# Kernel optimization log

Hardware: AMD Instinct MI355X
Metric: run time of the kernel (lower is better)

Reference implementation:

```python
import jax, jax.numpy as jnp
from jax import lax
import numpy as np


def _rnn_tanh_layer(x, W_ih, W_hh, b_ih, b_hh, return_seq):
    # x: [B, T, I]; W_ih: [H, I]; W_hh: [H, H]
    B = x.shape[0]
    H = W_hh.shape[0]
    # Precompute input projection for all timesteps (one big GEMM).
    xw = jnp.einsum('bti,hi->bth', x, W_ih) + b_ih + b_hh  # [B, T, H]
    xw_t = jnp.swapaxes(xw, 0, 1)  # [T, B, H] for scan
    h0 = jnp.zeros((B, H), dtype=x.dtype)

    def step(h, xt):
        h_new = jnp.tanh(xt + h @ W_hh.T)
        return h_new, (h_new if return_seq else None)

    hT, hs = lax.scan(step, h0, xw_t)
    if return_seq:
        return jnp.swapaxes(hs, 0, 1), hT  # [B, T, H], [B, H]
    return None, hT


def setup_inputs() -> dict:
    key = jax.random.key(0)
    ks = jax.random.split(key, 12)
    B, T, I, H1, H2, C = 512, 1024, 32, 128, 64, 10

    def unif(k, shape, fan):
        bound = 1.0 / np.sqrt(fan)
        return jax.random.uniform(k, shape, jnp.float32, -bound, bound)

    return {
        'x': jax.random.normal(ks[0], (B, T, I), jnp.float32),
        'W_ih1': unif(ks[1], (H1, I), H1),
        'W_hh1': unif(ks[2], (H1, H1), H1),
        'b_ih1': unif(ks[3], (H1,), H1),
        'b_hh1': unif(ks[4], (H1,), H1),
        'W_ih2': unif(ks[5], (H2, H1), H2),
        'W_hh2': unif(ks[6], (H2, H2), H2),
        'b_ih2': unif(ks[7], (H2,), H2),
        'b_hh2': unif(ks[8], (H2,), H2),
        'W_fc': unif(ks[9], (C, H2), H2),
        'b_fc': unif(ks[10], (C,), H2),
    }


def reference(x, W_ih1, W_hh1, b_ih1, b_hh1, W_ih2, W_hh2, b_ih2, b_hh2, W_fc, b_fc):
    out1, _h1 = _rnn_tanh_layer(x, W_ih1, W_hh1, b_ih1, b_hh1, return_seq=True)
    _none, h2 = _rnn_tanh_layer(out1, W_ih2, W_hh2, b_ih2, b_hh2, return_seq=False)
    # Dropout(p=0.3) is identity in eval mode.
    logits = h2 @ W_fc.T + b_fc  # [B, 10]
    return logits
```

## Files before the change

### kernel.cpp

```cpp
#include <hip/hip_runtime.h>
#include <stdint.h>


typedef _Float16 f16x8 __attribute__((ext_vector_type(8)));
typedef float f32x4 __attribute__((ext_vector_type(4)));

#define MFMA_F16(A, B, C) __builtin_amdgcn_mfma_f32_16x16x32_f16((A), (B), (C), 0, 0, 0)

__device__ __forceinline__ float tanh_fast(float x) {
  float t = __builtin_amdgcn_exp2f(x * 2.88539008177792681472f);
  return 1.0f - 2.0f * __builtin_amdgcn_rcpf(t + 1.0f);
}

__device__ __forceinline__ uint32_t pk16(float a, float b) {
  return __builtin_bit_cast(uint32_t, __builtin_amdgcn_cvt_pkrtz(a, b));
}

__global__ __launch_bounds__(256) void rnn_fused(
    const float* __restrict__ x,
    const float* __restrict__ Wih1, const float* __restrict__ Whh1,
    const float* __restrict__ bih1, const float* __restrict__ bhh1,
    const float* __restrict__ Wih2, const float* __restrict__ Whh2,
    const float* __restrict__ bih2, const float* __restrict__ bhh2,
    const float* __restrict__ Wfc,  const float* __restrict__ bfc,
    float* __restrict__ out)
{
  constexpr int T = 1024, I = 32, H1 = 128, H2 = 64, BB = 16;

  __shared__ __align__(16) unsigned char smem[16384];

  const int tid  = threadIdx.x;
  const int w    = tid >> 6;
  const int lane = tid & 63;
  const int g    = lane >> 4;
  const int n    = lane & 15;
  const int b0   = blockIdx.x * BB;

  {
    uint32_t* p = (uint32_t*)smem;
    for (int i = tid; i < 1024; i += 256) p[i] = 0u;
    uint32_t* q = (uint32_t*)(smem + 8192);
    for (int i = tid; i < 512; i += 256) q[i] = 0u;
  }

  auto cvt8 = [](const float* s) -> f16x8 {
    f16x8 r;
#pragma unroll
    for (int j = 0; j < 8; ++j) r[j] = (_Float16)s[j];
    return r;
  };

  f16x8 aU[2][4];
  f16x8 aI1[2];
  f16x8 aI2[4];
  f16x8 aR2[2];
#pragma unroll
  for (int ti = 0; ti < 2; ++ti) {
    const int ch = (2 * w + ti) * 16 + n;
#pragma unroll
    for (int k4 = 0; k4 < 4; ++k4)
      aU[ti][k4] = cvt8(Whh1 + ch * H1 + k4 * 32 + g * 8);
    aI1[ti] = cvt8(Wih1 + ch * I + g * 8);
  }
  {
    const int ch2 = w * 16 + n;
#pragma unroll
    for (int k4 = 0; k4 < 4; ++k4)
      aI2[k4] = cvt8(Wih2 + ch2 * H1 + k4 * 32 + g * 8);
#pragma unroll
    for (int k2 = 0; k2 < 2; ++k2)
      aR2[k2] = cvt8(Whh2 + ch2 * H2 + k2 * 32 + g * 8);
  }

  f32x4 bias1[2], bias2;
#pragma unroll
  for (int ti = 0; ti < 2; ++ti) {
    const int ch = (2 * w + ti) * 16 + g * 4;
#pragma unroll
    for (int r = 0; r < 4; ++r) bias1[ti][r] = bih1[ch + r] + bhh1[ch + r];
  }
  {
    const int ch2 = w * 16 + g * 4;
#pragma unroll
    for (int r = 0; r < 4; ++r) bias2[r] = bih2[ch2 + r] + bhh2[ch2 + r];
  }

  int roff1[4], roff2[2], woff1[2], woff2;
#pragma unroll
  for (int k4 = 0; k4 < 4; ++k4)
    roff1[k4] = n * 256 + (((k4 * 4 + g) ^ (n & 7)) << 4);
#pragma unroll
  for (int k2 = 0; k2 < 2; ++k2)
    roff2[k2] = n * 128 + (((k2 * 4 + g) ^ (n & 7)) << 4);
#pragma unroll
  for (int ti = 0; ti < 2; ++ti) {
    const int tt = 2 * w + ti;
    woff1[ti] = n * 256 + (((2 * tt + (g >> 1)) ^ (n & 7)) << 4) + (g & 1) * 8;
  }
  woff2 = n * 128 + (((2 * w + (g >> 1)) ^ (n & 7)) << 4) + (g & 1) * 8;

  const float* xp = x + (size_t)(b0 + n) * T * I + g * 8;
  f32x4 xrA0 = *(const f32x4*)(xp + 0 * I);
  f32x4 xrA1 = *(const f32x4*)(xp + 0 * I + 4);
  f32x4 xrB0 = *(const f32x4*)(xp + 1 * I);
  f32x4 xrB1 = *(const f32x4*)(xp + 1 * I + 4);

  __syncthreads();

  auto tanh_pack = [&](const f32x4& a, uint32_t& lo, uint32_t& hi) {
    const float v0 = tanh_fast(a[0]), v1 = tanh_fast(a[1]);
    const float v2 = tanh_fast(a[2]), v3 = tanh_fast(a[3]);
    lo = pk16(v0, v1);
    hi = pk16(v2, v3);
  };

  auto step = [&](int t, int cur, f32x4& xr0, f32x4& xr1) {
    f16x8 xf;
    {
      union { uint32_t u[4]; f16x8 v; } tmp;
      tmp.u[0] = pk16(xr0[0], xr0[1]);
      tmp.u[1] = pk16(xr0[2], xr0[3]);
      tmp.u[2] = pk16(xr1[0], xr1[1]);
      tmp.u[3] = pk16(xr1[2], xr1[3]);
      xf = tmp.v;
    }

    const char* H1c = (const char*)smem + cur * 4096;
    char*       H1n = (char*)smem + (cur ^ 1) * 4096;
    const char* H2r = (const char*)smem + 8192 + (cur ^ 1) * 2048;
    char*       H2w = (char*)smem + 8192 + cur * 2048;

    f16x8 b1[4];
#pragma unroll
    for (int k4 = 0; k4 < 4; ++k4)
      b1[k4] = *(const f16x8*)(H1c + roff1[k4]);

    f32x4 acc0 = bias1[0];
    f32x4 acc1 = bias1[1];
    acc0 = MFMA_F16(aI1[0], xf, acc0);
    acc1 = MFMA_F16(aI1[1], xf, acc1);
#pragma unroll
    for (int k4 = 0; k4 < 4; ++k4) {
      acc0 = MFMA_F16(aU[0][k4], b1[k4], acc0);
      acc1 = MFMA_F16(aU[1][k4], b1[k4], acc1);
    }

    if (t + 2 < T) {
      xr0 = *(const f32x4*)(xp + (t + 2) * I);
      xr1 = *(const f32x4*)(xp + (t + 2) * I + 4);
    }

    if (t > 0) {
      f16x8 b2[2];
#pragma unroll
      for (int k2 = 0; k2 < 2; ++k2)
        b2[k2] = *(const f16x8*)(H2r + roff2[k2]);
      f32x4 acc2 = bias2;
#pragma unroll
      for (int k4 = 0; k4 < 4; ++k4) acc2 = MFMA_F16(aI2[k4], b1[k4], acc2);
#pragma unroll
      for (int k2 = 0; k2 < 2; ++k2) acc2 = MFMA_F16(aR2[k2], b2[k2], acc2);
      uint32_t lo, hi;
      tanh_pack(acc2, lo, hi);
      *(uint2*)(H2w + woff2) = make_uint2(lo, hi);
    }

    {
      uint32_t lo, hi;
      tanh_pack(acc0, lo, hi);
      *(uint2*)(H1n + woff1[0]) = make_uint2(lo, hi);
      tanh_pack(acc1, lo, hi);
      *(uint2*)(H1n + woff1[1]) = make_uint2(lo, hi);
    }

    __syncthreads();
  };

  for (int t2 = 0; t2 < T; t2 += 2) {
    step(t2,     0, xrA0, xrA1);
    step(t2 + 1, 1, xrB0, xrB1);
  }

  {
    const char* H1c = (const char*)smem;
    const char* H2r = (const char*)smem + 8192 + 2048;
    f16x8 b1[4];
#pragma unroll
    for (int k4 = 0; k4 < 4; ++k4)
      b1[k4] = *(const f16x8*)(H1c + roff1[k4]);
    f16x8 b2[2];
#pragma unroll
    for (int k2 = 0; k2 < 2; ++k2)
      b2[k2] = *(const f16x8*)(H2r + roff2[k2]);
    f32x4 acc2 = bias2;
#pragma unroll
    for (int k4 = 0; k4 < 4; ++k4) acc2 = MFMA_F16(aI2[k4], b1[k4], acc2);
#pragma unroll
    for (int k2 = 0; k2 < 2; ++k2) acc2 = MFMA_F16(aR2[k2], b2[k2], acc2);

    f32x4 hv;
#pragma unroll
    for (int r = 0; r < 4; ++r) hv[r] = tanh_fast(acc2[r]);
    const int ch0 = w * 16 + g * 4;
    *(f32x4*)(smem + 12288 + n * 256 + ch0 * 4) = hv;
  }
  __syncthreads();

  if (tid < BB * 10) {
    const int b = tid / 10, c = tid % 10;
    const float* hrow = (const float*)(smem + 12288 + b * 256);
    float acc = bfc[c];
#pragma unroll 8
    for (int k = 0; k < 64; ++k) acc += hrow[k] * Wfc[c * 64 + k];
    out[(size_t)(b0 + b) * 10 + c] = acc;
  }
}

extern "C" void kernel_launch(void* const* d_in, const int* in_sizes, int n_in,
                              void* d_out, int out_size, void* d_ws, size_t ws_size,
                              hipStream_t stream) {
  const float* x    = (const float*)d_in[0];
  const float* Wih1 = (const float*)d_in[1];
  const float* Whh1 = (const float*)d_in[2];
  const float* bih1 = (const float*)d_in[3];
  const float* bhh1 = (const float*)d_in[4];
  const float* Wih2 = (const float*)d_in[5];
  const float* Whh2 = (const float*)d_in[6];
  const float* bih2 = (const float*)d_in[7];
  const float* bhh2 = (const float*)d_in[8];
  const float* Wfc  = (const float*)d_in[9];
  const float* bfc  = (const float*)d_in[10];

  hipLaunchKernelGGL(rnn_fused, dim3(512 / 16), dim3(256), 0, stream,
                     x, Wih1, Whh1, bih1, bhh1, Wih2, Whh2, bih2, bhh2,
                     Wfc, bfc, (float*)d_out);
}
```

Before: 515.1 us.

## Split layer-1 and layer-2 recurrences across warp-specialized wavefronts with lighter barriers

The block grows from 4 to 12 wavefronts. Eight wavefronts each own 16 layer-1 channels and four own 16 layer-2 channels, so each wave's serial MFMA chain per timestep is shorter. Each step now ends with a bare lgkmcnt wait plus s_barrier instead of __syncthreads. The accumulation is split into independent MFMA chains that are summed at the end, and the next timestep's input projection is computed ahead of time off the critical path. The cost is a barrier spanning three times as many waves and higher register/occupancy pressure from 768-thread blocks.

New measurement: 551.6 us. 7.1% more time.

```diff
diff --git a/kernel.cpp b/kernel.cpp
--- a/kernel.cpp
+++ b/kernel.cpp
@@ -16,7 +16,11 @@
   return __builtin_bit_cast(uint32_t, __builtin_amdgcn_cvt_pkrtz(a, b));
 }
 
-__global__ __launch_bounds__(256) void rnn_fused(
+__device__ __forceinline__ void sync_lds() {
+  asm volatile("s_waitcnt lgkmcnt(0)\n\ts_barrier" ::: "memory");
+}
+
+__global__ __launch_bounds__(768) void rnn_fused(
     const float* __restrict__ x,
     const float* __restrict__ Wih1, const float* __restrict__ Whh1,
     const float* __restrict__ bih1, const float* __restrict__ bhh1,
@@ -38,9 +42,9 @@
 
   {
     uint32_t* p = (uint32_t*)smem;
-    for (int i = tid; i < 1024; i += 256) p[i] = 0u;
+    for (int i = tid; i < 1024; i += 768) p[i] = 0u;
     uint32_t* q = (uint32_t*)(smem + 8192);
-    for (int i = tid; i < 512; i += 256) q[i] = 0u;
+    for (int i = tid; i < 512; i += 768) q[i] = 0u;
   }
 
   auto cvt8 = [](const float* s) -> f16x8 {
@@ -50,160 +54,149 @@
     return r;
   };
 
-  f16x8 aU[2][4];
-  f16x8 aI1[2];
-  f16x8 aI2[4];
-  f16x8 aR2[2];
-#pragma unroll
-  for (int ti = 0; ti < 2; ++ti) {
-    const int ch = (2 * w + ti) * 16 + n;
-#pragma unroll
-    for (int k4 = 0; k4 < 4; ++k4)
-      aU[ti][k4] = cvt8(Whh1 + ch * H1 + k4 * 32 + g * 8);
-    aI1[ti] = cvt8(Wih1 + ch * I + g * 8);
-  }
-  {
-    const int ch2 = w * 16 + n;
-#pragma unroll
-    for (int k4 = 0; k4 < 4; ++k4)
-      aI2[k4] = cvt8(Wih2 + ch2 * H1 + k4 * 32 + g * 8);
-#pragma unroll
-    for (int k2 = 0; k2 < 2; ++k2)
-      aR2[k2] = cvt8(Whh2 + ch2 * H2 + k2 * 32 + g * 8);
-  }
-
-  f32x4 bias1[2], bias2;
-#pragma unroll
-  for (int ti = 0; ti < 2; ++ti) {
-    const int ch = (2 * w + ti) * 16 + g * 4;
-#pragma unroll
-    for (int r = 0; r < 4; ++r) bias1[ti][r] = bih1[ch + r] + bhh1[ch + r];
-  }
-  {
-    const int ch2 = w * 16 + g * 4;
-#pragma unroll
-    for (int r = 0; r < 4; ++r) bias2[r] = bih2[ch2 + r] + bhh2[ch2 + r];
-  }
-
-  int roff1[4], roff2[2], woff1[2], woff2;
+  int roff1[4];
 #pragma unroll
   for (int k4 = 0; k4 < 4; ++k4)
     roff1[k4] = n * 256 + (((k4 * 4 + g) ^ (n & 7)) << 4);
-#pragma unroll
-  for (int k2 = 0; k2 < 2; ++k2)
-    roff2[k2] = n * 128 + (((k2 * 4 + g) ^ (n & 7)) << 4);
-#pragma unroll
-  for (int ti = 0; ti < 2; ++ti) {
-    const int tt = 2 * w + ti;
-    woff1[ti] = n * 256 + (((2 * tt + (g >> 1)) ^ (n & 7)) << 4) + (g & 1) * 8;
-  }
-  woff2 = n * 128 + (((2 * w + (g >> 1)) ^ (n & 7)) << 4) + (g & 1) * 8;
-
-  const float* xp = x + (size_t)(b0 + n) * T * I + g * 8;
-  f32x4 xrA0 = *(const f32x4*)(xp + 0 * I);
-  f32x4 xrA1 = *(const f32x4*)(xp + 0 * I + 4);
-  f32x4 xrB0 = *(const f32x4*)(xp + 1 * I);
-  f32x4 xrB1 = *(const f32x4*)(xp + 1 * I + 4);
 
   __syncthreads();
 
-  auto tanh_pack = [&](const f32x4& a, uint32_t& lo, uint32_t& hi) {
-    const float v0 = tanh_fast(a[0]), v1 = tanh_fast(a[1]);
-    const float v2 = tanh_fast(a[2]), v3 = tanh_fast(a[3]);
-    lo = pk16(v0, v1);
-    hi = pk16(v2, v3);
-  };
-
-  auto step = [&](int t, int cur, f32x4& xr0, f32x4& xr1) {
-    f16x8 xf;
+  if (w < 8) {
+    f16x8 aU[4], aI1;
+#pragma unroll
+    for (int k4 = 0; k4 < 4; ++k4)
+      aU[k4] = cvt8(Whh1 + (16 * w + n) * H1 + k4 * 32 + g * 8);
+    aI1 = cvt8(Wih1 + (16 * w + n) * I + g * 8);
+    f32x4 bias1;
+#pragma unroll
+    for (int r = 0; r < 4; ++r) bias1[r] = bih1[16 * w + g * 4 + r] + bhh1[16 * w + g * 4 + r];
+
+    const int woff = n * 256 + (((2 * w + (g >> 1)) ^ (n & 7)) << 4) + (g & 1) * 8;
+    const float* xp = x + (size_t)(b0 + n) * T * I + g * 8;
+
+    f32x4 q0a = *(const f32x4*)(xp + 0 * I), q0b = *(const f32x4*)(xp + 0 * I + 4);
+    f32x4 q1a = *(const f32x4*)(xp + 1 * I), q1b = *(const f32x4*)(xp + 1 * I + 4);
+    f32x4 q2a = *(const f32x4*)(xp + 2 * I), q2b = *(const f32x4*)(xp + 2 * I + 4);
+    f32x4 q3a = *(const f32x4*)(xp + 3 * I), q3b = *(const f32x4*)(xp + 3 * I + 4);
+
+    f32x4 accI;
     {
       union { uint32_t u[4]; f16x8 v; } tmp;
-      tmp.u[0] = pk16(xr0[0], xr0[1]);
-      tmp.u[1] = pk16(xr0[2], xr0[3]);
-      tmp.u[2] = pk16(xr1[0], xr1[1]);
-      tmp.u[3] = pk16(xr1[2], xr1[3]);
-      xf = tmp.v;
-    }
-
-    const char* H1c = (const char*)smem + cur * 4096;
-    char*       H1n = (char*)smem + (cur ^ 1) * 4096;
-    const char* H2r = (const char*)smem + 8192 + (cur ^ 1) * 2048;
-    char*       H2w = (char*)smem + 8192 + cur * 2048;
-
-    f16x8 b1[4];
+      tmp.u[0] = pk16(q0a[0], q0a[1]); tmp.u[1] = pk16(q0a[2], q0a[3]);
+      tmp.u[2] = pk16(q0b[0], q0b[1]); tmp.u[3] = pk16(q0b[2], q0b[3]);
+      accI = MFMA_F16(aI1, tmp.v, bias1);
+    }
+
+    auto stepL1 = [&](int t, int cur, f32x4& la, f32x4& lb,
+                      const f32x4& pa, const f32x4& pb) {
+      const char* H1c = (const char*)smem + cur * 4096;
+      char*       H1n = (char*)smem + (cur ^ 1) * 4096;
+      f16x8 b1k0 = *(const f16x8*)(H1c + roff1[0]);
+      f16x8 b1k1 = *(const f16x8*)(H1c + roff1[1]);
+      f16x8 b1k2 = *(const f16x8*)(H1c + roff1[2]);
+      f16x8 b1k3 = *(const f16x8*)(H1c + roff1[3]);
+      if (t + 4 < T) {
+        la = *(const f32x4*)(xp + (t + 4) * I);
+        lb = *(const f32x4*)(xp + (t + 4) * I + 4);
+      }
+      f32x4 zero = {0.f, 0.f, 0.f, 0.f};
+      f32x4 aA = MFMA_F16(aU[0], b1k0, accI);
+      f32x4 aB = MFMA_F16(aU[2], b1k2, zero);
+      aA = MFMA_F16(aU[1], b1k1, aA);
+      aB = MFMA_F16(aU[3], b1k3, aB);
+      {
+        union { uint32_t u[4]; f16x8 v; } tmp;
+        tmp.u[0] = pk16(pa[0], pa[1]); tmp.u[1] = pk16(pa[2], pa[3]);
+        tmp.u[2] = pk16(pb[0], pb[1]); tmp.u[3] = pk16(pb[2], pb[3]);
+        accI = MFMA_F16(aI1, tmp.v, bias1);
+      }
+      f32x4 s = aA + aB;
+      const uint32_t lo = pk16(tanh_fast(s[0]), tanh_fast(s[1]));
+      const uint32_t hi = pk16(tanh_fast(s[2]), tanh_fast(s[3]));
+      *(uint2*)(H1n + woff) = make_uint2(lo, hi);
+      sync_lds();
+    };
+
+    for (int t = 0; t < T; t += 4) {
+      stepL1(t + 0, 0, q0a, q0b, q1a, q1b);
+      stepL1(t + 1, 1, q1a, q1b, q2a, q2b);
+      stepL1(t + 2, 0, q2a, q2b, q3a, q3b);
+      stepL1(t + 3, 1, q3a, q3b, q0a, q0b);
+    }
+  } else {
+    const int j = w - 8;
+    f16x8 aI2[4], aR2[2];
 #pragma unroll
     for (int k4 = 0; k4 < 4; ++k4)
-      b1[k4] = *(const f16x8*)(H1c + roff1[k4]);
-
-    f32x4 acc0 = bias1[0];
-    f32x4 acc1 = bias1[1];
-    acc0 = MFMA_F16(aI1[0], xf, acc0);
-    acc1 = MFMA_F16(aI1[1], xf, acc1);
-#pragma unroll
-    for (int k4 = 0; k4 < 4; ++k4) {
-      acc0 = MFMA_F16(aU[0][k4], b1[k4], acc0);
-      acc1 = MFMA_F16(aU[1][k4], b1[k4], acc1);
-    }
-
-    if (t + 2 < T) {
-      xr0 = *(const f32x4*)(xp + (t + 2) * I);
-      xr1 = *(const f32x4*)(xp + (t + 2) * I + 4);
-    }
-
-    if (t > 0) {
-      f16x8 b2[2];
-#pragma unroll
-      for (int k2 = 0; k2 < 2; ++k2)
-        b2[k2] = *(const f16x8*)(H2r + roff2[k2]);
-      f32x4 acc2 = bias2;
-#pragma unroll
-      for (int k4 = 0; k4 < 4; ++k4) acc2 = MFMA_F16(aI2[k4], b1[k4], acc2);
-#pragma unroll
-      for (int k2 = 0; k2 < 2; ++k2) acc2 = MFMA_F16(aR2[k2], b2[k2], acc2);
-      uint32_t lo, hi;
-      tanh_pack(acc2, lo, hi);
-      *(uint2*)(H2w + woff2) = make_uint2(lo, hi);
+      aI2[k4] = cvt8(Wih2 + (16 * j + n) * H1 + k4 * 32 + g * 8);
+#pragma unroll
+    for (int k2 = 0; k2 < 2; ++k2)
+      aR2[k2] = cvt8(Whh2 + (16 * j + n) * H2 + k2 * 32 + g * 8);
+    f32x4 bias2;
+#pragma unroll
+    for (int r = 0; r < 4; ++r) bias2[r] = bih2[16 * j + g * 4 + r] + bhh2[16 * j + g * 4 + r];
+
+    int roff2[2];
+#pragma unroll
+    for (int k2 = 0; k2 < 2; ++k2)
+      roff2[k2] = n * 128 + (((k2 * 4 + g) ^ (n & 7)) << 4);
+    const int woff2 = n * 128 + (((2 * j + (g >> 1)) ^ (n & 7)) << 4) + (g & 1) * 8;
+
+    auto stepL2 = [&](int t, int cur) {
+      if (t > 0) {
+        const char* H1c = (const char*)smem + cur * 4096;
+        const char* H2r = (const char*)smem + 8192 + (cur ^ 1) * 2048;
+        char*       H2w = (char*)smem + 8192 + cur * 2048;
+        f16x8 b1k0 = *(const f16x8*)(H1c + roff1[0]);
+        f16x8 b1k1 = *(const f16x8*)(H1c + roff1[1]);
+        f16x8 b1k2 = *(const f16x8*)(H1c + roff1[2]);
+        f16x8 b1k3 = *(const f16x8*)(H1c + roff1[3]);
+        f16x8 b2k0 = *(const f16x8*)(H2r + roff2[0]);
+        f16x8 b2k1 = *(const f16x8*)(H2r + roff2[1]);
+        f32x4 zero = {0.f, 0.f, 0.f, 0.f};
+        f32x4 cA = MFMA_F16(aI2[0], b1k0, zero);
+        f32x4 cB = MFMA_F16(aI2[1], b1k1, zero);
+        f32x4 cC = MFMA_F16(aR2[0], b2k0, bias2);
+        cA = MFMA_F16(aI2[2], b1k2, cA);
+        cB = MFMA_F16(aI2[3], b1k3, cB);
+        cC = MFMA_F16(aR2[1], b2k1, cC);
+        f32x4 s = cA + cB + cC;
+        const uint32_t lo = pk16(tanh_fast(s[0]), tanh_fast(s[1]));
+        const uint32_t hi = pk16(tanh_fast(s[2]), tanh_fast(s[3]));
+        *(uint2*)(H2w + woff2) = make_uint2(lo, hi);
+      }
+      sync_lds();
+    };
+
+    for (int t = 0; t < T; t += 2) {
+      stepL2(t + 0, 0);
+      stepL2(t + 1, 1);
     }
 
     {
-      uint32_t lo, hi;
-      tanh_pack(acc0, lo, hi);
-      *(uint2*)(H1n + woff1[0]) = make_uint2(lo, hi);
-      tanh_pack(acc1, lo, hi);
-      *(uint2*)(H1n + woff1[1]) = make_uint2(lo, hi);
-    }
-
-    __syncthreads();
-  };
-
-  for (int t2 = 0; t2 < T; t2 += 2) {
-    step(t2,     0, xrA0, xrA1);
-    step(t2 + 1, 1, xrB0, xrB1);
+      const char* H1c = (const char*)smem;
+      const char* H2r = (const char*)smem + 8192 + 2048;
+      f16x8 b1k0 = *(const f16x8*)(H1c + roff1[0]);
+      f16x8 b1k1 = *(const f16x8*)(H1c + roff1[1]);
+      f16x8 b1k2 = *(const f16x8*)(H1c + roff1[2]);
+      f16x8 b1k3 = *(const f16x8*)(H1c + roff1[3]);
+      f16x8 b2k0 = *(const f16x8*)(H2r + roff2[0]);
+      f16x8 b2k1 = *(const f16x8*)(H2r + roff2[1]);
+      f32x4 zero = {0.f, 0.f, 0.f, 0.f};
+      f32x4 cA = MFMA_F16(aI2[0], b1k0, zero);
+      f32x4 cB = MFMA_F16(aI2[1], b1k1, zero);
+      f32x4 cC = MFMA_F16(aR2[0], b2k0, bias2);
+      cA = MFMA_F16(aI2[2], b1k2, cA);
+      cB = MFMA_F16(aI2[3], b1k3, cB);
+      cC = MFMA_F16(aR2[1], b2k1, cC);
+      f32x4 s = cA + cB + cC;
+      f32x4 hv;
+#pragma unroll
+      for (int r = 0; r < 4; ++r) hv[r] = tanh_fast(s[r]);
+      *(f32x4*)(smem + 12288 + n * 256 + (16 * j + 4 * g) * 4) = hv;
+    }
   }
 
-  {
-    const char* H1c = (const char*)smem;
-    const char* H2r = (const char*)smem + 8192 + 2048;
-    f16x8 b1[4];
-#pragma unroll
-    for (int k4 = 0; k4 < 4; ++k4)
-      b1[k4] = *(const f16x8*)(H1c + roff1[k4]);
-    f16x8 b2[2];
-#pragma unroll
-    for (int k2 = 0; k2 < 2; ++k2)
-      b2[k2] = *(const f16x8*)(H2r + roff2[k2]);
-    f32x4 acc2 = bias2;
-#pragma unroll
-    for (int k4 = 0; k4 < 4; ++k4) acc2 = MFMA_F16(aI2[k4], b1[k4], acc2);
-#pragma unroll
-    for (int k2 = 0; k2 < 2; ++k2) acc2 = MFMA_F16(aR2[k2], b2[k2], acc2);
-
-    f32x4 hv;
-#pragma unroll
-    for (int r = 0; r < 4; ++r) hv[r] = tanh_fast(acc2[r]);
-    const int ch0 = w * 16 + g * 4;
-    *(f32x4*)(smem + 12288 + n * 256 + ch0 * 4) = hv;
-  }
   __syncthreads();
 
   if (tid < BB * 10) {
@@ -231,7 +224,7 @@
   const float* Wfc  = (const float*)d_in[9];
   const float* bfc  = (const float*)d_in[10];
 
-  hipLaunchKernelGGL(rnn_fused, dim3(512 / 16), dim3(256), 0, stream,
+  hipLaunchKernelGGL(rnn_fused, dim3(512 / 16), dim3(768), 0, stream,
                      x, Wih1, Whh1, bih1, bhh1, Wih2, Whh2, bih2, bhh2,
                      Wfc, bfc, (float*)d_out);
 }
```

## Shorten RNN step critical path with split accumulators and precomputed input projection

Applied to the files above, without the earlier changes.

Restructures each recurrent step so the input projection for the next timestep is computed off the critical path, and splits the MFMA accumulation chains into two or three independent partial sums that are added at the end. This shortens the dependent MFMA chain per step. It also deepens the x prefetch to four steps, replaces __syncthreads with a raw lgkmcnt wait plus s_barrier, and vectorises the weight loads. The raw barrier skips the vmcnt wait, so it depends on the LDS-only ordering being sufficient, and it uses more registers.

Result: slower. 570.6 us (+10.8%).

```diff
diff --git a/kernel.cpp b/kernel.cpp
--- a/kernel.cpp
+++ b/kernel.cpp
@@ -14,6 +14,10 @@
 
 __device__ __forceinline__ uint32_t pk16(float a, float b) {
   return __builtin_bit_cast(uint32_t, __builtin_amdgcn_cvt_pkrtz(a, b));
+}
+
+__device__ __forceinline__ void sync_lds() {
+  asm volatile("s_waitcnt lgkmcnt(0)\n\ts_barrier" ::: "memory");
 }
 
 __global__ __launch_bounds__(256) void rnn_fused(
@@ -44,9 +48,11 @@
   }
 
   auto cvt8 = [](const float* s) -> f16x8 {
+    f32x4 a = *(const f32x4*)s;
+    f32x4 b = *(const f32x4*)(s + 4);
     f16x8 r;
 #pragma unroll
-    for (int j = 0; j < 8; ++j) r[j] = (_Float16)s[j];
+    for (int j = 0; j < 4; ++j) { r[j] = (_Float16)a[j]; r[4 + j] = (_Float16)b[j]; }
     return r;
   };
 
@@ -99,112 +105,127 @@
   }
   woff2 = n * 128 + (((2 * w + (g >> 1)) ^ (n & 7)) << 4) + (g & 1) * 8;
 
+  __syncthreads();
+
   const float* xp = x + (size_t)(b0 + n) * T * I + g * 8;
-  f32x4 xrA0 = *(const f32x4*)(xp + 0 * I);
-  f32x4 xrA1 = *(const f32x4*)(xp + 0 * I + 4);
-  f32x4 xrB0 = *(const f32x4*)(xp + 1 * I);
-  f32x4 xrB1 = *(const f32x4*)(xp + 1 * I + 4);
-
-  __syncthreads();
+  f32x4 q0a = *(const f32x4*)(xp + 0 * I), q0b = *(const f32x4*)(xp + 0 * I + 4);
+  f32x4 q1a = *(const f32x4*)(xp + 1 * I), q1b = *(const f32x4*)(xp + 1 * I + 4);
+  f32x4 q2a = *(const f32x4*)(xp + 2 * I), q2b = *(const f32x4*)(xp + 2 * I + 4);
+  f32x4 q3a = *(const f32x4*)(xp + 3 * I), q3b = *(const f32x4*)(xp + 3 * I + 4);
+
+  auto pack_x = [&](const f32x4& a, const f32x4& b) -> f16x8 {
+    union { uint32_t u[4]; f16x8 v; } tmp;
+    tmp.u[0] = pk16(a[0], a[1]); tmp.u[1] = pk16(a[2], a[3]);
+    tmp.u[2] = pk16(b[0], b[1]); tmp.u[3] = pk16(b[2], b[3]);
+    return tmp.v;
+  };
+
+  f32x4 accI0, accI1;
+  {
+    f16x8 xf = pack_x(q0a, q0b);
+    accI0 = MFMA_F16(aI1[0], xf, bias1[0]);
+    accI1 = MFMA_F16(aI1[1], xf, bias1[1]);
+  }
 
   auto tanh_pack = [&](const f32x4& a, uint32_t& lo, uint32_t& hi) {
-    const float v0 = tanh_fast(a[0]), v1 = tanh_fast(a[1]);
-    const float v2 = tanh_fast(a[2]), v3 = tanh_fast(a[3]);
-    lo = pk16(v0, v1);
-    hi = pk16(v2, v3);
-  };
-
-  auto step = [&](int t, int cur, f32x4& xr0, f32x4& xr1) {
-    f16x8 xf;
-    {
-      union { uint32_t u[4]; f16x8 v; } tmp;
-      tmp.u[0] = pk16(xr0[0], xr0[1]);
-      tmp.u[1] = pk16(xr0[2], xr0[3]);
-      tmp.u[2] = pk16(xr1[0], xr1[1]);
-      tmp.u[3] = pk16(xr1[2], xr1[3]);
-      xf = tmp.v;
-    }
-
+    lo = pk16(tanh_fast(a[0]), tanh_fast(a[1]));
+    hi = pk16(tanh_fast(a[2]), tanh_fast(a[3]));
+  };
+
+  auto step = [&](int t, int cur, f32x4& la, f32x4& lb,
+                  const f32x4& pa, const f32x4& pb) {
     const char* H1c = (const char*)smem + cur * 4096;
     char*       H1n = (char*)smem + (cur ^ 1) * 4096;
     const char* H2r = (const char*)smem + 8192 + (cur ^ 1) * 2048;
     char*       H2w = (char*)smem + 8192 + cur * 2048;
 
-    f16x8 b1[4];
-#pragma unroll
-    for (int k4 = 0; k4 < 4; ++k4)
-      b1[k4] = *(const f16x8*)(H1c + roff1[k4]);
-
-    f32x4 acc0 = bias1[0];
-    f32x4 acc1 = bias1[1];
-    acc0 = MFMA_F16(aI1[0], xf, acc0);
-    acc1 = MFMA_F16(aI1[1], xf, acc1);
-#pragma unroll
-    for (int k4 = 0; k4 < 4; ++k4) {
-      acc0 = MFMA_F16(aU[0][k4], b1[k4], acc0);
-      acc1 = MFMA_F16(aU[1][k4], b1[k4], acc1);
-    }
-
-    if (t + 2 < T) {
-      xr0 = *(const f32x4*)(xp + (t + 2) * I);
-      xr1 = *(const f32x4*)(xp + (t + 2) * I + 4);
-    }
-
-    if (t > 0) {
-      f16x8 b2[2];
-#pragma unroll
-      for (int k2 = 0; k2 < 2; ++k2)
-        b2[k2] = *(const f16x8*)(H2r + roff2[k2]);
-      f32x4 acc2 = bias2;
-#pragma unroll
-      for (int k4 = 0; k4 < 4; ++k4) acc2 = MFMA_F16(aI2[k4], b1[k4], acc2);
-#pragma unroll
-      for (int k2 = 0; k2 < 2; ++k2) acc2 = MFMA_F16(aR2[k2], b2[k2], acc2);
+    f16x8 b1k0 = *(const f16x8*)(H1c + roff1[0]);
+    f16x8 b1k1 = *(const f16x8*)(H1c + roff1[1]);
+    f16x8 b1k2 = *(const f16x8*)(H1c + roff1[2]);
+    f16x8 b1k3 = *(const f16x8*)(H1c + roff1[3]);
+    f16x8 b2k0 = *(const f16x8*)(H2r + roff2[0]);
+    f16x8 b2k1 = *(const f16x8*)(H2r + roff2[1]);
+
+    if (t + 4 < T) {
+      la = *(const f32x4*)(xp + (t + 4) * I);
+      lb = *(const f32x4*)(xp + (t + 4) * I + 4);
+    }
+
+    f32x4 zero = {0.f, 0.f, 0.f, 0.f};
+    f32x4 aA0 = MFMA_F16(aU[0][0], b1k0, accI0);
+    f32x4 aB0 = MFMA_F16(aU[0][2], b1k2, zero);
+    f32x4 aA1 = MFMA_F16(aU[1][0], b1k0, accI1);
+    f32x4 aB1 = MFMA_F16(aU[1][2], b1k2, zero);
+    aA0 = MFMA_F16(aU[0][1], b1k1, aA0);
+    aB0 = MFMA_F16(aU[0][3], b1k3, aB0);
+    aA1 = MFMA_F16(aU[1][1], b1k1, aA1);
+    aB1 = MFMA_F16(aU[1][3], b1k3, aB1);
+
+    f32x4 cA, cB, cC;
+    const bool do_l2 = (t > 0);
+    if (do_l2) {
+      cA = MFMA_F16(aI2[0], b1k0, bias2);
+      cB = MFMA_F16(aI2[1], b1k1, zero);
+      cC = MFMA_F16(aR2[0], b2k0, zero);
+      cA = MFMA_F16(aI2[2], b1k2, cA);
+      cB = MFMA_F16(aI2[3], b1k3, cB);
+      cC = MFMA_F16(aR2[1], b2k1, cC);
+    }
+
+    {
+      f16x8 xf = pack_x(pa, pb);
+      accI0 = MFMA_F16(aI1[0], xf, bias1[0]);
+      accI1 = MFMA_F16(aI1[1], xf, bias1[1]);
+    }
+
+    {
+      f32x4 s0 = aA0 + aB0, s1 = aA1 + aB1;
       uint32_t lo, hi;
-      tanh_pack(acc2, lo, hi);
+      tanh_pack(s0, lo, hi);
+      *(uint2*)(H1n + woff1[0]) = make_uint2(lo, hi);
+      tanh_pack(s1, lo, hi);
+      *(uint2*)(H1n + woff1[1]) = make_uint2(lo, hi);
+    }
+    if (do_l2) {
+      f32x4 s2 = cA + cB + cC;
+      uint32_t lo, hi;
+      tanh_pack(s2, lo, hi);
       *(uint2*)(H2w + woff2) = make_uint2(lo, hi);
     }
 
-    {
-      uint32_t lo, hi;
-      tanh_pack(acc0, lo, hi);
-      *(uint2*)(H1n + woff1[0]) = make_uint2(lo, hi);
-      tanh_pack(acc1, lo, hi);
-      *(uint2*)(H1n + woff1[1]) = make_uint2(lo, hi);
-    }
-
-    __syncthreads();
-  };
-
-  for (int t2 = 0; t2 < T; t2 += 2) {
-    step(t2,     0, xrA0, xrA1);
-    step(t2 + 1, 1, xrB0, xrB1);
+    sync_lds();
+  };
+
+  for (int t = 0; t < T; t += 4) {
+    step(t + 0, 0, q0a, q0b, q1a, q1b);
+    step(t + 1, 1, q1a, q1b, q2a, q2b);
+    step(t + 2, 0, q2a, q2b, q3a, q3b);
+    step(t + 3, 1, q3a, q3b, q0a, q0b);
   }
 
   {
     const char* H1c = (const char*)smem;
     const char* H2r = (const char*)smem + 8192 + 2048;
-    f16x8 b1[4];
-#pragma unroll
-    for (int k4 = 0; k4 < 4; ++k4)
-      b1[k4] = *(const f16x8*)(H1c + roff1[k4]);
-    f16x8 b2[2];
-#pragma unroll
-    for (int k2 = 0; k2 < 2; ++k2)
-      b2[k2] = *(const f16x8*)(H2r + roff2[k2]);
-    f32x4 acc2 = bias2;
-#pragma unroll
-    for (int k4 = 0; k4 < 4; ++k4) acc2 = MFMA_F16(aI2[k4], b1[k4], acc2);
-#pragma unroll
-    for (int k2 = 0; k2 < 2; ++k2) acc2 = MFMA_F16(aR2[k2], b2[k2], acc2);
-
+    f16x8 b1k0 = *(const f16x8*)(H1c + roff1[0]);
+    f16x8 b1k1 = *(const f16x8*)(H1c + roff1[1]);
+    f16x8 b1k2 = *(const f16x8*)(H1c + roff1[2]);
+    f16x8 b1k3 = *(const f16x8*)(H1c + roff1[3]);
+    f16x8 b2k0 = *(const f16x8*)(H2r + roff2[0]);
+    f16x8 b2k1 = *(const f16x8*)(H2r + roff2[1]);
+    f32x4 zero = {0.f, 0.f, 0.f, 0.f};
+    f32x4 cA = MFMA_F16(aI2[0], b1k0, bias2);
+    f32x4 cB = MFMA_F16(aI2[1], b1k1, zero);
+    f32x4 cC = MFMA_F16(aR2[0], b2k0, zero);
+    cA = MFMA_F16(aI2[2], b1k2, cA);
+    cB = MFMA_F16(aI2[3], b1k3, cB);
+    cC = MFMA_F16(aR2[1], b2k1, cC);
+    f32x4 s = cA + cB + cC;
     f32x4 hv;
 #pragma unroll
-    for (int r = 0; r < 4; ++r) hv[r] = tanh_fast(acc2[r]);
-    const int ch0 = w * 16 + g * 4;
-    *(f32x4*)(smem + 12288 + n * 256 + ch0 * 4) = hv;
-  }
-  __syncthreads();
+    for (int r = 0; r < 4; ++r) hv[r] = tanh_fast(s[r]);
+    *(f32x4*)(smem + 12288 + n * 256 + (16 * w + 4 * g) * 4) = hv;
+  }
+  sync_lds();
 
   if (tid < BB * 10) {
     const int b = tid / 10, c = tid % 10;
```
